# Performance work log

Hardware: AMD Instinct MI355X
Metric: run time of the kernel (lower is better)

The kernel has to match this reference:

```python
import jax, jax.numpy as jnp
import numpy as np

NUM_HEADS = 32
NUM_KV_HEADS = 8
HEAD_DIM = 128
HIDDEN = 4096
ROPE_THETA = 10000.0
SLIDING_WINDOW = 1024
NEG_INF = -1e9


def _make_sliding_window_mask(q_len, kv_len, window):
    # additive mask: 0 where attendable (causal AND within window), -inf otherwise
    i = jnp.arange(q_len)[:, None]
    j = jnp.arange(kv_len)[None, :]
    allowed = (j <= i) & (j > i - window)
    return jnp.where(allowed, 0.0, NEG_INF).astype(jnp.float32)[None, None]  # [1,1,q,kv]


def _rope_tables(seq_len, head_dim, theta):
    inv_freq = 1.0 / (theta ** (jnp.arange(0, head_dim, 2, dtype=jnp.float32) / head_dim))
    t = jnp.arange(seq_len, dtype=jnp.float32)
    freqs = jnp.einsum('i,j->ij', t, inv_freq)        # [S, D/2]
    emb = jnp.concatenate([freqs, freqs], axis=-1)     # [S, D]
    return jnp.cos(emb), jnp.sin(emb)


def _rotate_half(x):
    d = x.shape[-1] // 2
    return jnp.concatenate([-x[..., d:], x[..., :d]], axis=-1)


def setup_inputs() -> dict:
    key = jax.random.key(0)
    ks = jax.random.split(key, 5)
    B, S = 1, 2048
    sc = 0.02
    hidden_states = jax.random.normal(ks[0], (B, S, HIDDEN), dtype=jnp.float32)
    Wq = jax.random.normal(ks[1], (HIDDEN, NUM_HEADS * HEAD_DIM), dtype=jnp.float32) * sc
    Wk = jax.random.normal(ks[2], (HIDDEN, NUM_KV_HEADS * HEAD_DIM), dtype=jnp.float32) * sc
    Wv = jax.random.normal(ks[3], (HIDDEN, NUM_KV_HEADS * HEAD_DIM), dtype=jnp.float32) * sc
    Wo = jax.random.normal(ks[4], (NUM_HEADS * HEAD_DIM, HIDDEN), dtype=jnp.float32) * sc
    attention_mask = _make_sliding_window_mask(S, S, SLIDING_WINDOW)
    position_ids = jnp.arange(S, dtype=jnp.int64)[None, :]
    return {"hidden_states": hidden_states, "attention_mask": attention_mask,
            "position_ids": position_ids, "Wq": Wq, "Wk": Wk, "Wv": Wv, "Wo": Wo}


def reference(hidden_states, attention_mask, position_ids, Wq, Wk, Wv, Wo):
    B, S, _ = hidden_states.shape
    # projections
    q = (hidden_states @ Wq).reshape(B, S, NUM_HEADS, HEAD_DIM).transpose(0, 2, 1, 3)      # [B,H,S,D]
    k = (hidden_states @ Wk).reshape(B, S, NUM_KV_HEADS, HEAD_DIM).transpose(0, 2, 1, 3)   # [B,Hk,S,D]
    v = (hidden_states @ Wv).reshape(B, S, NUM_KV_HEADS, HEAD_DIM).transpose(0, 2, 1, 3)
    # RoPE
    cos_t, sin_t = _rope_tables(S, HEAD_DIM, ROPE_THETA)
    cos = cos_t[position_ids][:, None]  # [B,1,S,D]
    sin = sin_t[position_ids][:, None]
    q = q * cos + _rotate_half(q) * sin
    k = k * cos + _rotate_half(k) * sin
    # repeat_kv (GQA): [B,Hk,S,D] -> [B,H,S,D]
    n_rep = NUM_HEADS // NUM_KV_HEADS
    k = jnp.repeat(k, n_rep, axis=1)
    v = jnp.repeat(v, n_rep, axis=1)
    # attention
    scores = jnp.einsum('bhqd,bhkd->bhqk', q, k) / np.sqrt(HEAD_DIM)
    scores = scores + attention_mask
    probs = jax.nn.softmax(scores, axis=-1)
    out = jnp.einsum('bhqk,bhkd->bhqd', probs, v)
    out = out.transpose(0, 2, 1, 3).reshape(B, S, HIDDEN)
    return out @ Wo
```

## Files before the change

### kernel.cpp

```cpp
#include <hip/hip_runtime.h>

typedef __attribute__((ext_vector_type(8))) short short8;
typedef __attribute__((ext_vector_type(4))) short s16x4;
typedef __attribute__((ext_vector_type(4))) float f32x4;
typedef unsigned short u16;
typedef unsigned int u32;

__device__ __forceinline__ u16 f2bf(float f) {
  union { float f; unsigned int u; } v; v.f = f;
  unsigned int r = (v.u + 0x7FFFu + ((v.u >> 16) & 1u)) >> 16;
  return (u16)r;
}
__device__ __forceinline__ float bf2f(u16 b) {
  union { unsigned int u; float f; } v; v.u = ((unsigned int)b) << 16;
  return v.f;
}
__device__ __forceinline__ void load_lds16(const void* g, void* l) {
  __builtin_amdgcn_global_load_lds((const __attribute__((address_space(1))) void*)g,
                                   (__attribute__((address_space(3))) void*)l, 16, 0, 0);
}

__global__ void cvt_f32_bf16_kernel(const float* __restrict__ in, u16* __restrict__ out, int n4) {
  int i = blockIdx.x * blockDim.x + threadIdx.x;
  if (i >= n4) return;
  float4 v = ((const float4*)in)[i];
  ushort4 o;
  o.x = f2bf(v.x); o.y = f2bf(v.y); o.z = f2bf(v.z); o.w = f2bf(v.w);
  ((ushort4*)out)[i] = o;
}

__global__ void combine2_f32_kernel(float* __restrict__ out, const u16* __restrict__ p0,
                                    const u16* __restrict__ p1, int n8) {
  int i = blockIdx.x * blockDim.x + threadIdx.x;
  if (i >= n8) return;
  short8 a = ((const short8*)p0)[i];
  short8 b = ((const short8*)p1)[i];
  float4 o0, o1;
  o0.x = bf2f((u16)a[0]) + bf2f((u16)b[0]);
  o0.y = bf2f((u16)a[1]) + bf2f((u16)b[1]);
  o0.z = bf2f((u16)a[2]) + bf2f((u16)b[2]);
  o0.w = bf2f((u16)a[3]) + bf2f((u16)b[3]);
  o1.x = bf2f((u16)a[4]) + bf2f((u16)b[4]);
  o1.y = bf2f((u16)a[5]) + bf2f((u16)b[5]);
  o1.z = bf2f((u16)a[6]) + bf2f((u16)b[6]);
  o1.w = bf2f((u16)a[7]) + bf2f((u16)b[7]);
  ((float4*)out)[i * 2]     = o0;
  ((float4*)out)[i * 2 + 1] = o1;
}

__global__ void combine_kv_kernel(const u16* __restrict__ PKV, u16* __restrict__ Kb,
                                  u16* __restrict__ Vt) {
  int i = blockIdx.x * blockDim.x + threadIdx.x;
  const u16* src; u16* dst; size_t off;
  if (i < 262144) { off = (size_t)i; dst = Kb; src = PKV; }
  else            { off = (size_t)(i - 262144); dst = Vt; src = PKV + 2097152; }
  float s[8] = {0.f, 0.f, 0.f, 0.f, 0.f, 0.f, 0.f, 0.f};
#pragma unroll
  for (int z = 0; z < 4; ++z) {
    short8 v = *(const short8*)(src + (size_t)z * 4194304 + off * 8);
#pragma unroll
    for (int j = 0; j < 8; ++j) s[j] += bf2f((u16)v[j]);
  }
  short8 o;
#pragma unroll
  for (int j = 0; j < 8; ++j) o[j] = (short)f2bf(s[j]);
  ((short8*)dst)[off] = o;
}

__device__ __forceinline__ void tconv64_tile(const float* __restrict__ W, u16* __restrict__ Wt,
                                             int K, int N, int nb, int kb, int tid) {
  __shared__ float tile[64][65];
  int tx = tid & 15, ty = tid >> 4;
  const float* src = W + (size_t)(kb + ty) * N + nb + tx * 4;
#pragma unroll
  for (int i = 0; i < 4; ++i) {
    float4 v = *(const float4*)(src + (size_t)i * 16 * N);
    tile[ty + i * 16][tx * 4 + 0] = v.x;
    tile[ty + i * 16][tx * 4 + 1] = v.y;
    tile[ty + i * 16][tx * 4 + 2] = v.z;
    tile[ty + i * 16][tx * 4 + 3] = v.w;
  }
  __syncthreads();
  u16* dst = Wt + (size_t)(nb + ty) * K + kb + tx * 4;
#pragma unroll
  for (int i = 0; i < 4; ++i) {
    s16x4 o;
#pragma unroll
    for (int j = 0; j < 4; ++j) o[j] = (short)f2bf(tile[tx * 4 + j][ty + i * 16]);
    *(s16x4*)(dst + (size_t)i * 16 * K) = o;
  }
}

__global__ void tconv3_kernel(const float* __restrict__ Wq, const float* __restrict__ Wk,
                              const float* __restrict__ Wv, u16* __restrict__ WqT,
                              u16* __restrict__ WkvT) {
  int id = blockIdx.x;
  if (id < 4096)      tconv64_tile(Wq, WqT, 4096, 4096, (id & 63) * 64, (id >> 6) * 64, threadIdx.x);
  else if (id < 5120) { int t = id - 4096; tconv64_tile(Wk, WkvT, 4096, 1024, (t & 15) * 64, (t >> 4) * 64, threadIdx.x); }
  else                { int t = id - 5120; tconv64_tile(Wv, WkvT + (size_t)1024 * 4096, 4096, 1024, (t & 15) * 64, (t >> 4) * 64, threadIdx.x); }
}

__global__ void tconv1_kernel(const float* __restrict__ W, u16* __restrict__ Wt) {
  int id = blockIdx.x;
  tconv64_tile(W, Wt, 4096, 4096, (id & 63) * 64, (id >> 6) * 64, threadIdx.x);
}

__global__ void rope_kernel(u16* __restrict__ Qb, const u16* __restrict__ Qp1, u16* __restrict__ Kb) {
  int idx = blockIdx.x * blockDim.x + threadIdx.x;
  int j, t, hh, s;
  if (idx < 4194304) {
    j = idx & 63; t = idx >> 6; hh = t & 31; s = t >> 5;
    float invf = exp2f(-(float)j * (13.287712379549449f / 64.0f));
    float ang = (float)s * invf;
    float sn, cs;
    sincosf(ang, &sn, &cs);
    size_t base = (size_t)s * 4096 + hh * 128 + j;
    u16* p = Qb + base;
    const u16* p1 = Qp1 + base;
    float a = bf2f(p[0]) + bf2f(p1[0]);
    float b = bf2f(p[64]) + bf2f(p1[64]);
    const float scale = 0.12751781828987514f;
    p[0]  = f2bf((a * cs - b * sn) * scale);
    p[64] = f2bf((b * cs + a * sn) * scale);
  } else {
    int id = idx - 4194304;
    j = id & 63; t = id >> 6; hh = t & 7; s = t >> 3;
    float invf = exp2f(-(float)j * (13.287712379549449f / 64.0f));
    float ang = (float)s * invf;
    float sn, cs;
    sincosf(ang, &sn, &cs);
    u16* p = Kb + (size_t)s * 1024 + hh * 128 + j;
    float a = bf2f(p[0]), b = bf2f(p[64]);
    p[0]  = f2bf(a * cs - b * sn);
    p[64] = f2bf(b * cs + a * sn);
  }
}

template<int KVEPI>
__global__ __launch_bounds__(512, 1) void gemm8p_kernel(
    const u16* __restrict__ A, const u16* __restrict__ B,
    u16* __restrict__ C0, u16* __restrict__ C1, int N, int K, int KH) {
  __shared__ u16 Sh[2][2][2][8192];
  int tid = threadIdx.x, lane = tid & 63, wid = tid >> 6;
  int wr = wid >> 2, wc = wid & 3;
  int g = lane >> 4, q = lane & 15;
  int id = blockIdx.z * gridDim.x * gridDim.y + blockIdx.y * gridDim.x + blockIdx.x;
  int tot = gridDim.x * gridDim.y * gridDim.z;
  int swz = (id & 7) * (tot >> 3) + (id >> 3);
  int perh = gridDim.x * gridDim.y;
  int z = swz / perh, rem = swz % perh;
  int m0 = (rem / gridDim.x) * 256, n0 = (rem % gridDim.x) * 256;
  int k0 = z * KH;
  f32x4 acc[8][4];
#pragma unroll
  for (int i = 0; i < 8; ++i)
#pragma unroll
    for (int j = 0; j < 4; ++j) acc[i][j] = (f32x4){0.f, 0.f, 0.f, 0.f};
  int srow = tid >> 2;
  int scol = (tid & 3) * 8;
  const u16* ga = A + (size_t)(m0 + srow) * K + k0 + scol;
  const u16* gb = B + (size_t)(n0 + srow) * K + k0 + scol;
  int arow = wr * 128 + q;
  int brow = wc * 64 + q;
  int nt = KH >> 6;

  auto stageH = [&](int b, int mat, int h, int t) {
    const u16* gp = (mat ? gb : ga) + t * 64 + h * 32;
    char* dst = (char*)&Sh[b][mat][h][0];
#pragma unroll
    for (int it = 0; it < 2; ++it)
      load_lds16(gp + (size_t)it * 128 * K, dst + it * 8192 + tid * 16);
  };
  auto readA = [&](int b, int h, int fb, short8 (&af)[4]) {
    const u16* s = &Sh[b][0][h][0];
#pragma unroll
    for (int m = 0; m < 4; ++m)
      af[m] = *(const short8*)&s[(arow + (fb + m) * 16) * 32 + g * 8];
  };
  auto readB = [&](int b, int h, short8 (&bf)[4]) {
    const u16* s = &Sh[b][1][h][0];
#pragma unroll
    for (int n = 0; n < 4; ++n)
      bf[n] = *(const short8*)&s[(brow + n * 16) * 32 + g * 8];
  };

  stageH(0, 0, 0, 0); stageH(0, 1, 0, 0);
  stageH(0, 0, 1, 0); stageH(0, 1, 1, 0);
  stageH(1, 0, 0, 1); stageH(1, 1, 0, 1);
  asm volatile("s_waitcnt vmcnt(4)" ::: "memory");
  __builtin_amdgcn_s_barrier();

#define PHASE(FB)                                                        \
  __builtin_amdgcn_s_barrier();                                          \
  asm volatile("s_waitcnt lgkmcnt(0)" ::: "memory");                     \
  __builtin_amdgcn_sched_barrier(0);                                     \
  __builtin_amdgcn_s_setprio(1);                                         \
  _Pragma("unroll")                                                      \
  for (int m = 0; m < 4; ++m)                                            \
    _Pragma("unroll")                                                    \
    for (int n = 0; n < 4; ++n)                                          \
      acc[FB + m][n] = __builtin_amdgcn_mfma_f32_16x16x32_bf16(          \
          af[m], bf[n], acc[FB + m][n], 0, 0, 0);                        \
  __builtin_amdgcn_s_setprio(0);                                         \
  __builtin_amdgcn_s_barrier();

  for (int t = 0; t < nt; t += 2) {
    bool s2 = (t + 2 < nt);
    short8 af[4], bf[4];
    readA(0, 0, 0, af); readB(0, 0, bf);
    stageH(1, 0, 1, t + 1);
    PHASE(0)
    readA(0, 0, 4, af);
    stageH(1, 1, 1, t + 1);
    PHASE(4)
    readA(0, 1, 0, af); readB(0, 1, bf);
    if (s2) stageH(0, 0, 0, t + 2);
    PHASE(0)
    readA(0, 1, 4, af);
    if (s2) stageH(0, 1, 0, t + 2);
    PHASE(4)
    readA(1, 0, 0, af); readB(1, 0, bf);
    if (s2) { stageH(0, 0, 1, t + 2); asm volatile("s_waitcnt vmcnt(6)" ::: "memory"); }
    else    { asm volatile("s_waitcnt vmcnt(0)" ::: "memory"); }
    PHASE(0)
    readA(1, 0, 4, af);
    if (s2) stageH(0, 1, 1, t + 2);
    PHASE(4)
    readA(1, 1, 0, af); readB(1, 1, bf);
    if (s2) stageH(1, 0, 0, t + 3);
    PHASE(0)
    readA(1, 1, 4, af);
    if (s2) { stageH(1, 1, 0, t + 3); asm volatile("s_waitcnt vmcnt(4)" ::: "memory"); }
    PHASE(4)
  }
#undef PHASE

  int crow = m0 + wr * 128 + g * 4;
  int ccol = n0 + wc * 64 + q;
  if (KVEPI) {
    u16* Kpart = C0 + (size_t)z * 4194304;
    u16* Vpart = Kpart + 2097152;
    if (n0 < 1024) {
#pragma unroll
      for (int fm = 0; fm < 8; ++fm)
#pragma unroll
        for (int fn = 0; fn < 4; ++fn)
#pragma unroll
          for (int r = 0; r < 4; ++r)
            Kpart[(size_t)(crow + fm * 16 + r) * 1024 + ccol + fn * 16] = f2bf(acc[fm][fn][r]);
    } else {
#pragma unroll
      for (int fn = 0; fn < 4; ++fn) {
        int vcol = ccol + fn * 16 - 1024;
#pragma unroll
        for (int fm = 0; fm < 8; ++fm) {
          s16x4 o;
#pragma unroll
          for (int r = 0; r < 4; ++r) o[r] = (short)f2bf(acc[fm][fn][r]);
          *(s16x4*)(Vpart + (size_t)vcol * 2048 + crow + fm * 16) = o;
        }
      }
    }
  } else {
    u16* dst = z ? C1 : C0;
#pragma unroll
    for (int fm = 0; fm < 8; ++fm)
#pragma unroll
      for (int fn = 0; fn < 4; ++fn)
#pragma unroll
        for (int r = 0; r < 4; ++r)
          dst[(size_t)(crow + fm * 16 + r) * N + ccol + fn * 16] = f2bf(acc[fm][fn][r]);
  }
}

__global__ __launch_bounds__(512, 4) void attn_kernel(
    const u16* __restrict__ Q, const u16* __restrict__ Kg,
    const u16* __restrict__ Vt, u16* __restrict__ O) {
  __shared__ u16 Ks[2][64 * 128];
  __shared__ u16 Vs[2][128 * 64];
  int tid = threadIdx.x, lane = tid & 63, w = tid >> 6;
  int wg = w >> 2;
  int g = lane >> 4, q = lane & 15;
  int q0 = blockIdx.x * 128;
  int h = blockIdx.y, hk = h >> 2;
  int qbase = q0 + wg * 64;
  int qrow = qbase + (w & 3) * 16;
  int xorm = (lane & 7) << 3;
  short8 qf[4];
  {
    const u16* qp = Q + (size_t)(qrow + q) * 4096 + h * 128 + g * 8;
#pragma unroll
    for (int kk = 0; kk < 4; ++kk) qf[kk] = *(const short8*)(qp + kk * 32);
  }
  float mrow = -1e30f, lsum = 0.f;
  f32x4 of[8];
#pragma unroll
  for (int d = 0; d < 8; ++d) of[d] = (f32x4){0.f, 0.f, 0.f, 0.f};
  int bjt_lo = (q0 >= 1024) ? ((q0 - 1023) >> 6) : 0;
  int bjt_hi = (q0 + 64) >> 6;
  int wjt_lo = (qbase >= 1024) ? ((qbase - 1023) >> 6) : 0;
  int wjt_hi = qbase >> 6;
  int krow = tid >> 4;
  int kchunk = (tid & 15) ^ (krow & 7);
  const u16* kbase = Kg + (size_t)krow * 1024 + hk * 128 + (kchunk << 3);
  int vrow = tid >> 3;
  int vchunk = (tid & 7) ^ (vrow & 7);
  const u16* vbase = Vt + (size_t)(hk * 128 + vrow) * 2048 + (vchunk << 3);

  auto stageK = [&](int buf, int j0) {
    const u16* gp = kbase + (size_t)j0 * 1024;
#pragma unroll
    for (int it = 0; it < 2; ++it)
      load_lds16(gp + (size_t)it * 32 * 1024, (char*)(&Ks[buf][0]) + it * 8192 + tid * 16);
  };
  auto stageV = [&](int buf, int j0) {
    const u16* gp = vbase + j0;
#pragma unroll
    for (int it = 0; it < 2; ++it)
      load_lds16(gp + (size_t)it * 64 * 2048, (char*)(&Vs[buf][0]) + it * 8192 + tid * 16);
  };

  int cur = 0;
  stageK(0, bjt_lo << 6);
  stageV(0, bjt_lo << 6);
  asm volatile("s_waitcnt vmcnt(0)" ::: "memory");
  __syncthreads();
  for (int jt = bjt_lo; jt <= bjt_hi; ++jt) {
    int j0 = jt << 6;
    if (jt < bjt_hi) { stageK(cur ^ 1, j0 + 64); stageV(cur ^ 1, j0 + 64); }
    if (jt >= wjt_lo && jt <= wjt_hi) {
      f32x4 sf[4];
#pragma unroll
      for (int nt = 0; nt < 4; ++nt) sf[nt] = (f32x4){0.f, 0.f, 0.f, 0.f};
      const u16* ks = &Ks[cur][0];
      __builtin_amdgcn_s_setprio(1);
#pragma unroll
      for (int kk = 0; kk < 4; ++kk) {
        short8 qv = qf[kk];
        int col = (kk * 32 + g * 8) ^ xorm;
#pragma unroll
        for (int nt = 0; nt < 4; ++nt) {
          short8 kf = *(const short8*)&ks[(nt * 16 + q) * 128 + col];
          sf[nt] = __builtin_amdgcn_mfma_f32_16x16x32_bf16(kf, qv, sf[nt], 0, 0, 0);
        }
      }
      __builtin_amdgcn_s_setprio(0);
      float p[4][4];
#pragma unroll
      for (int nt = 0; nt < 4; ++nt)
#pragma unroll
        for (int r = 0; r < 4; ++r) p[nt][r] = sf[nt][r];
      if (j0 + 63 > qrow || j0 + 1009 <= qrow) {
        int qq = qrow + q;
        int kb = j0 + g * 4;
#pragma unroll
        for (int nt = 0; nt < 4; ++nt)
#pragma unroll
          for (int r = 0; r < 4; ++r) {
            int key = kb + nt * 16 + r;
            if (key > qq || key + 1024 <= qq) p[nt][r] = -1e9f;
          }
      }
      float tm = p[0][0];
#pragma unroll
      for (int nt = 0; nt < 4; ++nt)
#pragma unroll
        for (int r = 0; r < 4; ++r) tm = fmaxf(tm, p[nt][r]);
      tm = fmaxf(tm, __shfl_xor(tm, 16));
      tm = fmaxf(tm, __shfl_xor(tm, 32));
      if (__any(tm > mrow + 8.f)) {
        float nm = fmaxf(mrow, tm);
        float sc = __builtin_amdgcn_exp2f(mrow - nm);
        mrow = nm;
        lsum *= sc;
#pragma unroll
        for (int d = 0; d < 8; ++d) of[d] *= sc;
      }
      float ps = 0.f;
#pragma unroll
      for (int nt = 0; nt < 4; ++nt)
#pragma unroll
        for (int r = 0; r < 4; ++r) {
          float e = __builtin_amdgcn_exp2f(p[nt][r] - mrow);
          p[nt][r] = e;
          ps += e;
        }
      ps += __shfl_xor(ps, 16);
      ps += __shfl_xor(ps, 32);
      lsum += ps;
      u32 pk[4][2];
#pragma unroll
      for (int nt = 0; nt < 4; ++nt) {
        pk[nt][0] = __builtin_amdgcn_perm(__float_as_uint(p[nt][1]), __float_as_uint(p[nt][0]), 0x07060302u);
        pk[nt][1] = __builtin_amdgcn_perm(__float_as_uint(p[nt][3]), __float_as_uint(p[nt][2]), 0x07060302u);
      }
      int s0 = q + ((g & 1) ? 32 : 0);
      int s1 = s0 + 16;
      bool hi_sel = g >= 2;
      const u16* vs = &Vs[cur][0];
      __builtin_amdgcn_s_setprio(1);
#pragma unroll
      for (int kh = 0; kh < 2; ++kh) {
        int lo = kh * 2, hi = lo + 1;
        u32 a0 = (u32)__shfl((int)pk[lo][0], s0);
        u32 a1 = (u32)__shfl((int)pk[lo][1], s0);
        u32 b0 = (u32)__shfl((int)pk[hi][0], s0);
        u32 b1 = (u32)__shfl((int)pk[hi][1], s0);
        u32 a2 = (u32)__shfl((int)pk[lo][0], s1);
        u32 a3 = (u32)__shfl((int)pk[lo][1], s1);
        u32 b2 = (u32)__shfl((int)pk[hi][0], s1);
        u32 b3 = (u32)__shfl((int)pk[hi][1], s1);
        union { u32 u[4]; short8 s; } pb;
        pb.u[0] = hi_sel ? b0 : a0;
        pb.u[1] = hi_sel ? b1 : a1;
        pb.u[2] = hi_sel ? b2 : a2;
        pb.u[3] = hi_sel ? b3 : a3;
        int col = (kh * 32 + g * 8) ^ xorm;
#pragma unroll
        for (int dt = 0; dt < 8; ++dt) {
          short8 vv = *(const short8*)&vs[(dt * 16 + q) * 64 + col];
          of[dt] = __builtin_amdgcn_mfma_f32_16x16x32_bf16(vv, pb.s, of[dt], 0, 0, 0);
        }
      }
      __builtin_amdgcn_s_setprio(0);
    }
    asm volatile("s_waitcnt vmcnt(0)" ::: "memory");
    __builtin_amdgcn_s_barrier();
    cur ^= 1;
  }
  float inv = 1.f / lsum;
  u16* op = O + (size_t)(qrow + q) * 4096 + h * 128 + g * 4;
#pragma unroll
  for (int dt = 0; dt < 8; ++dt) {
    s16x4 o4;
#pragma unroll
    for (int r = 0; r < 4; ++r) o4[r] = (short)f2bf(of[dt][r] * inv);
    *(s16x4*)(op + dt * 16) = o4;
  }
}

extern "C" void kernel_launch(void* const* d_in, const int* in_sizes, int n_in,
                              void* d_out, int out_size, void* d_ws, size_t ws_size,
                              hipStream_t stream) {
  (void)in_sizes; (void)n_in; (void)out_size;
  const float* hs = (const float*)d_in[0];
  const float* Wq = (const float*)d_in[3];
  const float* Wk = (const float*)d_in[4];
  const float* Wv = (const float*)d_in[5];
  const float* Wo = (const float*)d_in[6];
  float* out = (float*)d_out;
  char* ws = (char*)d_ws;

  u16* Xb   = (u16*)(ws + 0);
  u16* Wt   = (u16*)(ws + 16777216);
  u16* WkvT = (u16*)(ws + 50331648);
  u16* Qb   = (u16*)(ws + 67108864);
  u16* Kb   = (u16*)(ws + 83886080);
  u16* Vtb  = (u16*)(ws + 88080384);
  u16* Ab   = (u16*)(ws + 96468992);
  u16* P1q  = Ab;
  u16* PKV  = Wt;
  u16* P0o  = WkvT;
  u16* P1o  = Qb;
  if (ws_size < 113246208u) return;

  cvt_f32_bf16_kernel<<<dim3(2097152 / 256), 256, 0, stream>>>(hs, Xb, 2097152);

  tconv3_kernel<<<dim3(6144), 256, 0, stream>>>(Wq, Wk, Wv, Wt, WkvT);

  gemm8p_kernel<0><<<dim3(16, 8, 2), 512, 0, stream>>>(Xb, Wt, Qb, P1q, 4096, 4096, 2048);

  gemm8p_kernel<1><<<dim3(8, 8, 4), 512, 0, stream>>>(Xb, WkvT, PKV, nullptr, 2048, 4096, 1024);
  combine_kv_kernel<<<dim3(2048), 256, 0, stream>>>(PKV, Kb, Vtb);

  rope_kernel<<<dim3(20480), 256, 0, stream>>>(Qb, P1q, Kb);

  attn_kernel<<<dim3(16, 32), 512, 0, stream>>>(Qb, Kb, Vtb, Ab);

  tconv1_kernel<<<dim3(4096), 256, 0, stream>>>(Wo, Wt);
  gemm8p_kernel<0><<<dim3(16, 8, 2), 512, 0, stream>>>(Ab, Wt, P0o, P1o, 4096, 4096, 2048);
  combine2_f32_kernel<<<dim3(4096), 256, 0, stream>>>(out, P0o, P1o, 1048576);
}
```

Baseline: 326.6 us.

## Swizzle LDS tile layout in GEMM and retime vmcnt waits per half-stage

Applies an XOR swizzle to the 16-byte chunk column used when staging A/B tiles into LDS and when reading MFMA fragments, so lanes of a wave reading different rows hit different LDS banks. It also moves the vmcnt waits to just after each compute phase, with looser counts, so the wait covers the half-tile that is read next rather than stalling earlier. The aim is to cut LDS bank conflicts and let more global loads stay in flight. The risk is that a wrong wait count leaves a race on LDS data, since the correctness of the counts is not obvious.

```diff
diff --git a/kernel.cpp b/kernel.cpp
--- a/kernel.cpp
+++ b/kernel.cpp
@@ -157,9 +157,10 @@
 #pragma unroll
     for (int j = 0; j < 4; ++j) acc[i][j] = (f32x4){0.f, 0.f, 0.f, 0.f};
   int srow = tid >> 2;
-  int scol = (tid & 3) * 8;
+  int scol = (((tid & 3) ^ ((tid >> 3) & 3)) << 3);
   const u16* ga = A + (size_t)(m0 + srow) * K + k0 + scol;
   const u16* gb = B + (size_t)(n0 + srow) * K + k0 + scol;
+  int rchunk = (g ^ ((q >> 1) & 3)) << 3;
   int arow = wr * 128 + q;
   int brow = wc * 64 + q;
   int nt = KH >> 6;
@@ -175,22 +176,22 @@
     const u16* s = &Sh[b][0][h][0];
 #pragma unroll
     for (int m = 0; m < 4; ++m)
-      af[m] = *(const short8*)&s[(arow + (fb + m) * 16) * 32 + g * 8];
+      af[m] = *(const short8*)&s[(arow + (fb + m) * 16) * 32 + rchunk];
   };
   auto readB = [&](int b, int h, short8 (&bf)[4]) {
     const u16* s = &Sh[b][1][h][0];
 #pragma unroll
     for (int n = 0; n < 4; ++n)
-      bf[n] = *(const short8*)&s[(brow + n * 16) * 32 + g * 8];
+      bf[n] = *(const short8*)&s[(brow + n * 16) * 32 + rchunk];
   };
 
   stageH(0, 0, 0, 0); stageH(0, 1, 0, 0);
   stageH(0, 0, 1, 0); stageH(0, 1, 1, 0);
   stageH(1, 0, 0, 1); stageH(1, 1, 0, 1);
-  asm volatile("s_waitcnt vmcnt(4)" ::: "memory");
+  asm volatile("s_waitcnt vmcnt(8)" ::: "memory");
   __builtin_amdgcn_s_barrier();
 
-#define PHASE(FB)                                                        \
+#define PHASEA(FB)                                                       \
   __builtin_amdgcn_s_barrier();                                          \
   asm volatile("s_waitcnt lgkmcnt(0)" ::: "memory");                     \
   __builtin_amdgcn_sched_barrier(0);                                     \
@@ -201,39 +202,51 @@
     for (int n = 0; n < 4; ++n)                                          \
       acc[FB + m][n] = __builtin_amdgcn_mfma_f32_16x16x32_bf16(          \
           af[m], bf[n], acc[FB + m][n], 0, 0, 0);                        \
-  __builtin_amdgcn_s_setprio(0);                                         \
-  __builtin_amdgcn_s_barrier();
+  __builtin_amdgcn_s_setprio(0);
 
   for (int t = 0; t < nt; t += 2) {
     bool s2 = (t + 2 < nt);
     short8 af[4], bf[4];
     readA(0, 0, 0, af); readB(0, 0, bf);
     stageH(1, 0, 1, t + 1);
-    PHASE(0)
+    PHASEA(0)
+    __builtin_amdgcn_s_barrier();
     readA(0, 0, 4, af);
     stageH(1, 1, 1, t + 1);
-    PHASE(4)
+    PHASEA(4)
+    asm volatile("s_waitcnt vmcnt(8)" ::: "memory");
+    __builtin_amdgcn_s_barrier();
     readA(0, 1, 0, af); readB(0, 1, bf);
     if (s2) stageH(0, 0, 0, t + 2);
-    PHASE(0)
+    PHASEA(0)
+    __builtin_amdgcn_s_barrier();
     readA(0, 1, 4, af);
     if (s2) stageH(0, 1, 0, t + 2);
-    PHASE(4)
+    PHASEA(4)
+    if (s2) { asm volatile("s_waitcnt vmcnt(8)" ::: "memory"); }
+    else    { asm volatile("s_waitcnt vmcnt(4)" ::: "memory"); }
+    __builtin_amdgcn_s_barrier();
     readA(1, 0, 0, af); readB(1, 0, bf);
-    if (s2) { stageH(0, 0, 1, t + 2); asm volatile("s_waitcnt vmcnt(6)" ::: "memory"); }
-    else    { asm volatile("s_waitcnt vmcnt(0)" ::: "memory"); }
-    PHASE(0)
+    if (s2) stageH(0, 0, 1, t + 2);
+    PHASEA(0)
+    __builtin_amdgcn_s_barrier();
     readA(1, 0, 4, af);
     if (s2) stageH(0, 1, 1, t + 2);
-    PHASE(4)
+    PHASEA(4)
+    if (s2) { asm volatile("s_waitcnt vmcnt(8)" ::: "memory"); }
+    else    { asm volatile("s_waitcnt vmcnt(0)" ::: "memory"); }
+    __builtin_amdgcn_s_barrier();
     readA(1, 1, 0, af); readB(1, 1, bf);
     if (s2) stageH(1, 0, 0, t + 3);
-    PHASE(0)
+    PHASEA(0)
+    __builtin_amdgcn_s_barrier();
     readA(1, 1, 4, af);
-    if (s2) { stageH(1, 1, 0, t + 3); asm volatile("s_waitcnt vmcnt(4)" ::: "memory"); }
-    PHASE(4)
-  }
-#undef PHASE
+    if (s2) stageH(1, 1, 0, t + 3);
+    PHASEA(4)
+    if (s2) { asm volatile("s_waitcnt vmcnt(8)" ::: "memory"); }
+    __builtin_amdgcn_s_barrier();
+  }
+#undef PHASEA
 
   int crow = m0 + wr * 128 + g * 4;
   int ccol = n0 + wc * 64 + q;
```

After: 321.7 us. Within noise of the previous version (-1.5%).
